# Kernel optimization log

Measured on AMD Instinct MI355X. Metric: run time of the kernel, lower is better.

## Reference

```python
import jax, jax.numpy as jnp
import numpy as np

WIRES = 4
DIM = 16  # 2**WIRES
EPS = 1e-5


def _rot_matrix(phi, theta, omega):
    # PennyLane Rot = RZ(omega) RY(theta) RZ(phi)
    c = jnp.cos(theta / 2).astype(jnp.complex64)
    s = jnp.sin(theta / 2).astype(jnp.complex64)
    ep = jnp.exp(-0.5j * (phi + omega).astype(jnp.complex64))
    em = jnp.exp(0.5j * (phi - omega).astype(jnp.complex64))
    m00 = ep * c
    m01 = -em * s
    m10 = jnp.conj(em) * s
    m11 = jnp.conj(ep) * c
    return jnp.stack([jnp.stack([m00, m01]), jnp.stack([m10, m11])])


def _apply_1q(state4, U, w):
    # state4: (B,2,2,2,2); apply 2x2 unitary on wire w (axis w+1)
    st = jnp.moveaxis(state4, w + 1, -1)
    st = st @ U.T  # sum_j st[...,j] * U[i,j]
    return jnp.moveaxis(st, -1, w + 1)


def _cnot_perm(c, t):
    # permutation of 16 basis indices for CNOT(control=c, target=t); wire 0 = MSB
    idx = np.arange(DIM)
    cbit = (idx >> (WIRES - 1 - c)) & 1
    return idx ^ (cbit << (WIRES - 1 - t))


def _circuit(x16, params):
    # AmplitudeEmbedding with normalize=True
    B = x16.shape[0]
    nrm = jnp.linalg.norm(x16, axis=1, keepdims=True)
    state = (x16 / nrm).astype(jnp.complex64)  # (B,16)
    L = params.shape[0]
    for l in range(L):
        st4 = state.reshape(B, 2, 2, 2, 2)
        for w in range(WIRES):
            U = _rot_matrix(params[l, w, 0], params[l, w, 1], params[l, w, 2])
            st4 = _apply_1q(st4, U, w)
        state = st4.reshape(B, DIM)
        r = (l % (WIRES - 1)) + 1  # StronglyEntanglingLayers default range
        for w in range(WIRES):
            perm = _cnot_perm(w, (w + r) % WIRES)
            state = state[:, perm]
    probs = (state.real ** 2 + state.imag ** 2)  # (B,16)
    p4 = probs.reshape(B, 2, 2, 2, 2)
    # <Z_w> = P(bit_w=0) - P(bit_w=1)
    outs = []
    for w in range(WIRES):
        axes = tuple(a for a in range(1, 5) if a != w + 1)
        pw = p4.sum(axis=axes)  # (B,2)
        outs.append(pw[:, 0] - pw[:, 1])
    return jnp.stack(outs, axis=1)  # (B,4)


def setup_inputs() -> dict:
    key = jax.random.key(0)
    k1, k2 = jax.random.split(key)
    B = 65536
    x = jax.random.normal(k1, (B, 1, 24, 24), dtype=jnp.float32)
    params = jax.random.normal(k2, (2, WIRES, 3), dtype=jnp.float32)
    gamma = jnp.ones((WIRES,), dtype=jnp.float32)
    beta = jnp.zeros((WIRES,), dtype=jnp.float32)
    return {"x": x, "params": params, "gamma": gamma, "beta": beta}


def reference(x, params, gamma, beta):
    B = x.shape[0]
    # avg_pool2d kernel 6: (B,1,24,24) -> (B,1,4,4) -> (B,16)
    pooled = x.reshape(B, 1, 4, 6, 4, 6).mean(axis=(3, 5)).reshape(B, DIM)
    out = _circuit(pooled, params)  # (B,4)
    # BatchNorm1d in training mode (biased batch stats)
    mu = out.mean(axis=0)
    var = ((out - mu) ** 2).mean(axis=0)
    return (out - mu) / jnp.sqrt(var + EPS) * gamma + beta
```

## Files before the change

### kernel.cpp

```cpp
#include <hip/hip_runtime.h>
#include <math.h>

#define BATCH 65536
#define XPER  576
#define NBLK  1024
#define EPB   64
#define GPI   16
#define ITERS (EPB / GPI)


__global__ __launch_bounds__(256) void circuit_kernel(
        const float* __restrict__ x, const float* __restrict__ params,
        float* __restrict__ out, float* __restrict__ accums) {
    __shared__ float sx[GPI * XPER];
    __shared__ float sU[512];
    __shared__ float sg[48];
    __shared__ float spart[8];

    const int t = threadIdx.x;
    const int e = t >> 4;
    const int p = t & 15;

    if (t < 8) {
        spart[t] = 0.0f;
        float phi   = params[t * 3 + 0];
        float theta = params[t * 3 + 1];
        float omega = params[t * 3 + 2];
        float apo = 0.5f * (phi + omega), amo = 0.5f * (phi - omega);
        sg[t * 6 + 0] = cosf(0.5f * theta);
        sg[t * 6 + 1] = sinf(0.5f * theta);
        sg[t * 6 + 2] = cosf(apo);
        sg[t * 6 + 3] = -sinf(apo);
        sg[t * 6 + 4] = cosf(amo);
        sg[t * 6 + 5] = sinf(amo);
    }
    __syncthreads();

    if (t < 16) {
        const int j = t;
        float Mr[16], Mi[16];
#pragma unroll
        for (int i = 0; i < 16; ++i) { Mr[i] = (i == j) ? 1.0f : 0.0f; Mi[i] = 0.0f; }

#pragma unroll
        for (int l = 0; l < 2; ++l) {
#pragma unroll
            for (int w = 0; w < 4; ++w) {
                const int g = l * 4 + w;
                float c   = sg[g * 6 + 0], s   = sg[g * 6 + 1];
                float epr = sg[g * 6 + 2], epi = sg[g * 6 + 3];
                float emr = sg[g * 6 + 4], emi = sg[g * 6 + 5];
                float m00r =  epr * c, m00i =  epi * c;
                float m01r = -emr * s, m01i = -emi * s;
                float m10r =  emr * s, m10i = -emi * s;
                float m11r =  epr * c, m11i = -epi * c;
                const int mask = 1 << (3 - w);
#pragma unroll
                for (int i = 0; i < 16; ++i) {
                    if (i & mask) continue;
                    int i1 = i | mask;
                    float r0 = Mr[i],  q0 = Mi[i];
                    float r1 = Mr[i1], q1 = Mi[i1];
                    Mr[i]  = m00r * r0 - m00i * q0 + m01r * r1 - m01i * q1;
                    Mi[i]  = m00r * q0 + m00i * r0 + m01r * q1 + m01i * r1;
                    Mr[i1] = m10r * r0 - m10i * q0 + m11r * r1 - m11i * q1;
                    Mi[i1] = m10r * q0 + m10i * r0 + m11r * q1 + m11i * r1;
                }
            }
            const int r = (l % 3) + 1;
#pragma unroll
            for (int w = 0; w < 4; ++w) {
                int tq = (w + r) & 3;
                int cb = 3 - w, tb = 3 - tq;
#pragma unroll
                for (int i = 0; i < 16; ++i) {
                    int pi = i ^ (((i >> cb) & 1) << tb);
                    if (pi > i) {
                        float tr = Mr[i]; Mr[i] = Mr[pi]; Mr[pi] = tr;
                        float ti = Mi[i]; Mi[i] = Mi[pi]; Mi[pi] = ti;
                    }
                }
            }
        }
#pragma unroll
        for (int i = 0; i < 16; ++i) {
            sU[i * 16 + j]       = Mr[i];
            sU[256 + i * 16 + j] = Mi[i];
        }
    }
    __syncthreads();

    float ur[16], ui[16];
    {
        const float4* u4 = (const float4*)(sU + p * 16);
        const float4* v4 = (const float4*)(sU + 256 + p * 16);
#pragma unroll
        for (int q = 0; q < 4; ++q) {
            float4 a = u4[q], b = v4[q];
            ur[4 * q + 0] = a.x; ur[4 * q + 1] = a.y; ur[4 * q + 2] = a.z; ur[4 * q + 3] = a.w;
            ui[4 * q + 0] = b.x; ui[4 * q + 1] = b.y; ui[4 * q + 2] = b.z; ui[4 * q + 3] = b.w;
        }
    }

    int c = -1;
    if      (p == 8) c = 0;
    else if (p == 4) c = 1;
    else if (p == 2) c = 2;
    else if (p == 1) c = 3;

    float accz = 0.0f, accz2 = 0.0f;
    const int base = blockIdx.x * EPB;

    for (int it = 0; it < ITERS; ++it) {
        const int ebase = base + it * GPI;
        const float4* src = (const float4*)(x + (size_t)ebase * XPER);
        float4* dst = (float4*)sx;
#pragma unroll
        for (int k = 0; k < 9; ++k) dst[k * 256 + t] = src[k * 256 + t];
        __syncthreads();

        const int r0 = (p >> 2) * 6, c0 = (p & 3) * 6;
        const float* bs = sx + e * XPER + r0 * 24 + c0;
        float sum = 0.0f;
#pragma unroll
        for (int i = 0; i < 6; ++i)
#pragma unroll
            for (int jj = 0; jj < 6; ++jj) sum += bs[i * 24 + jj];
        float v = sum * (1.0f / 36.0f);

        float n2 = v * v;
        n2 += __shfl_xor(n2, 1);
        n2 += __shfl_xor(n2, 2);
        n2 += __shfl_xor(n2, 4);
        n2 += __shfl_xor(n2, 8);

        float sr = 0.0f, si = 0.0f;
#pragma unroll
        for (int j = 0; j < 16; ++j) {
            float vj = __shfl(v, j, 16);
            sr = fmaf(ur[j], vj, sr);
            si = fmaf(ui[j], vj, si);
        }
        float prob = (sr * sr + si * si) / n2;

        float a = prob, o;
        o = __shfl_xor(a, 1); a = (t & 1) ? (o - a) : (a + o);
        o = __shfl_xor(a, 2); a = (t & 2) ? (o - a) : (a + o);
        o = __shfl_xor(a, 4); a = (t & 4) ? (o - a) : (a + o);
        o = __shfl_xor(a, 8); a = (t & 8) ? (o - a) : (a + o);

        if (c >= 0) {
            out[(size_t)(ebase + e) * 4 + c] = a;
            accz  += a;
            accz2 += a * a;
        }
        __syncthreads();
    }

    if (c >= 0) {
        atomicAdd(&spart[c], accz);
        atomicAdd(&spart[4 + c], accz2);
    }
    __syncthreads();
    if (t < 8) atomicAdd(&accums[t], spart[t]);
}

__global__ __launch_bounds__(256) void bn_apply(float* __restrict__ out,
                                                const float* __restrict__ accums,
                                                const float* __restrict__ gamma,
                                                const float* __restrict__ beta) {
    __shared__ float sc[8];
    const int t = threadIdx.x;
    if (t < 4) {
        float mu  = accums[t] * (1.0f / BATCH);
        float var = accums[4 + t] * (1.0f / BATCH) - mu * mu;
        float a = gamma[t] * rsqrtf(var + 1e-5f);
        sc[t]     = a;
        sc[4 + t] = beta[t] - mu * a;
    }
    __syncthreads();
    int i = blockIdx.x * 256 + t;
    float4 z = ((float4*)out)[i];
    z.x = fmaf(z.x, sc[0], sc[4]);
    z.y = fmaf(z.y, sc[1], sc[5]);
    z.z = fmaf(z.z, sc[2], sc[6]);
    z.w = fmaf(z.w, sc[3], sc[7]);
    ((float4*)out)[i] = z;
}

extern "C" void kernel_launch(void* const* d_in, const int* in_sizes, int n_in,
                              void* d_out, int out_size, void* d_ws, size_t ws_size,
                              hipStream_t stream) {
    const float* x      = (const float*)d_in[0];
    const float* params = (const float*)d_in[1];
    const float* gamma  = (const float*)d_in[2];
    const float* beta   = (const float*)d_in[3];
    float* out = (float*)d_out;
    float* ws  = (float*)d_ws;

    hipMemsetAsync(ws, 0, 8 * sizeof(float), stream);
    hipLaunchKernelGGL(circuit_kernel, dim3(NBLK), dim3(256), 0, stream,
                       x, params, out, ws);
    hipLaunchKernelGGL(bn_apply, dim3(BATCH / 256), dim3(256), 0, stream,
                       out, ws, gamma, beta);
}
```

Baseline: 44.97 us.

## Pool directly from global memory, 8 lanes per image, drop memset via per-block slots

Drops the shared-memory staging of input images and the per-iteration block barriers. Each lane now reads its two 6x6 pooling patches straight from global memory with float4 loads, and 8 lanes cooperate per image, each computing two rows of the 16x16 unitary product. Pooled values are exchanged through a small per-wave shared buffer instead of shuffles. BatchNorm statistics are written to per-block slots and reduced inside bn_apply, which removes the memset and the global atomics but adds a 1024-slot reduction in every bn_apply block.

```diff
diff --git a/kernel.cpp b/kernel.cpp
--- a/kernel.cpp
+++ b/kernel.cpp
@@ -4,22 +4,27 @@
 #define BATCH 65536
 #define XPER  576
 #define NBLK  1024
-#define EPB   64
-#define GPI   16
-#define ITERS (EPB / GPI)
-
-
-__global__ __launch_bounds__(256) void circuit_kernel(
+#define WPB   4
+#define RPW   2
+#define IPR   8
+
+
+__global__ __launch_bounds__(256, 3) void circuit_kernel(
         const float* __restrict__ x, const float* __restrict__ params,
-        float* __restrict__ out, float* __restrict__ accums) {
-    __shared__ float sx[GPI * XPER];
-    __shared__ float sU[512];
+        float* __restrict__ out, float* __restrict__ slots) {
+    __shared__ float sUr[16 * 20];
+    __shared__ float sUi[16 * 20];
     __shared__ float sg[48];
+    __shared__ float sv[WPB][IPR * 20];
     __shared__ float spart[8];
 
-    const int t = threadIdx.x;
-    const int e = t >> 4;
-    const int p = t & 15;
+    const int t    = threadIdx.x;
+    const int wid  = t >> 6;
+    const int lane = t & 63;
+    const int e    = lane >> 3;
+    const int q    = lane & 7;
+    const int pr   = q >> 1;
+    const int P    = q & 1;
 
     if (t < 8) {
         spart[t] = 0.0f;
@@ -41,7 +46,6 @@
         float Mr[16], Mi[16];
 #pragma unroll
         for (int i = 0; i < 16; ++i) { Mr[i] = (i == j) ? 1.0f : 0.0f; Mi[i] = 0.0f; }
-
 #pragma unroll
         for (int l = 0; l < 2; ++l) {
 #pragma unroll
@@ -67,10 +71,10 @@
                     Mi[i1] = m10r * q0 + m10i * r0 + m11r * q1 + m11i * r1;
                 }
             }
-            const int r = (l % 3) + 1;
+            const int rr = (l % 3) + 1;
 #pragma unroll
             for (int w = 0; w < 4; ++w) {
-                int tq = (w + r) & 3;
+                int tq = (w + rr) & 3;
                 int cb = 3 - w, tb = 3 - tq;
 #pragma unroll
                 for (int i = 0; i < 16; ++i) {
@@ -84,77 +88,90 @@
         }
 #pragma unroll
         for (int i = 0; i < 16; ++i) {
-            sU[i * 16 + j]       = Mr[i];
-            sU[256 + i * 16 + j] = Mi[i];
-        }
-    }
-    __syncthreads();
-
-    float ur[16], ui[16];
+            sUr[i * 20 + j] = Mr[i];
+            sUi[i * 20 + j] = Mi[i];
+        }
+    }
+    __syncthreads();
+
+    float u0r[16], u0i[16], u1r[16], u1i[16];
     {
-        const float4* u4 = (const float4*)(sU + p * 16);
-        const float4* v4 = (const float4*)(sU + 256 + p * 16);
-#pragma unroll
-        for (int q = 0; q < 4; ++q) {
-            float4 a = u4[q], b = v4[q];
-            ur[4 * q + 0] = a.x; ur[4 * q + 1] = a.y; ur[4 * q + 2] = a.z; ur[4 * q + 3] = a.w;
-            ui[4 * q + 0] = b.x; ui[4 * q + 1] = b.y; ui[4 * q + 2] = b.z; ui[4 * q + 3] = b.w;
+        const float4* r0 = (const float4*)(sUr + (2 * q) * 20);
+        const float4* r1 = (const float4*)(sUr + (2 * q + 1) * 20);
+        const float4* i0 = (const float4*)(sUi + (2 * q) * 20);
+        const float4* i1 = (const float4*)(sUi + (2 * q + 1) * 20);
+#pragma unroll
+        for (int m = 0; m < 4; ++m) {
+            float4 a = r0[m], b = r1[m], cc = i0[m], d = i1[m];
+            u0r[4*m+0]=a.x; u0r[4*m+1]=a.y; u0r[4*m+2]=a.z; u0r[4*m+3]=a.w;
+            u1r[4*m+0]=b.x; u1r[4*m+1]=b.y; u1r[4*m+2]=b.z; u1r[4*m+3]=b.w;
+            u0i[4*m+0]=cc.x; u0i[4*m+1]=cc.y; u0i[4*m+2]=cc.z; u0i[4*m+3]=cc.w;
+            u1i[4*m+0]=d.x; u1i[4*m+1]=d.y; u1i[4*m+2]=d.z; u1i[4*m+3]=d.w;
         }
     }
 
     int c = -1;
-    if      (p == 8) c = 0;
-    else if (p == 4) c = 1;
-    else if (p == 2) c = 2;
-    else if (p == 1) c = 3;
-
+    if      (q == 4) c = 0;
+    else if (q == 2) c = 1;
+    else if (q == 1) c = 2;
+    else if (q == 0) c = 3;
+
+    const int cbase = pr * 144 + P * 12;
     float accz = 0.0f, accz2 = 0.0f;
-    const int base = blockIdx.x * EPB;
-
-    for (int it = 0; it < ITERS; ++it) {
-        const int ebase = base + it * GPI;
-        const float4* src = (const float4*)(x + (size_t)ebase * XPER);
-        float4* dst = (float4*)sx;
-#pragma unroll
-        for (int k = 0; k < 9; ++k) dst[k * 256 + t] = src[k * 256 + t];
-        __syncthreads();
-
-        const int r0 = (p >> 2) * 6, c0 = (p & 3) * 6;
-        const float* bs = sx + e * XPER + r0 * 24 + c0;
-        float sum = 0.0f;
-#pragma unroll
-        for (int i = 0; i < 6; ++i)
-#pragma unroll
-            for (int jj = 0; jj < 6; ++jj) sum += bs[i * 24 + jj];
-        float v = sum * (1.0f / 36.0f);
-
-        float n2 = v * v;
-        n2 += __shfl_xor(n2, 1);
-        n2 += __shfl_xor(n2, 2);
-        n2 += __shfl_xor(n2, 4);
-        n2 += __shfl_xor(n2, 8);
-
-        float sr = 0.0f, si = 0.0f;
+
+#pragma unroll
+    for (int rd = 0; rd < RPW; ++rd) {
+        const size_t img = (size_t)blockIdx.x * 64 + wid * 16 + rd * 8 + e;
+        const float* ip = x + img * XPER + cbase;
+
+        float L = 0.0f, R = 0.0f;
+#pragma unroll
+        for (int r = 0; r < 6; ++r) {
+            float4 a = *(const float4*)(ip + r * 24);
+            float4 b = *(const float4*)(ip + r * 24 + 4);
+            float4 d = *(const float4*)(ip + r * 24 + 8);
+            L += a.x + a.y + a.z + a.w + b.x + b.y;
+            R += b.z + b.w + d.x + d.y + d.z + d.w;
+        }
+        float vL = L * (1.0f / 36.0f), vR = R * (1.0f / 36.0f);
+
+        *(float2*)(&sv[wid][e * 20 + 2 * q]) = make_float2(vL, vR);
+        float vv[16];
+        {
+            const float4* vb = (const float4*)(&sv[wid][e * 20]);
+#pragma unroll
+            for (int m = 0; m < 4; ++m) {
+                float4 a = vb[m];
+                vv[4*m+0]=a.x; vv[4*m+1]=a.y; vv[4*m+2]=a.z; vv[4*m+3]=a.w;
+            }
+        }
+
+        float n2 = 0.0f, sr0 = 0.0f, si0 = 0.0f, sr1 = 0.0f, si1 = 0.0f;
 #pragma unroll
         for (int j = 0; j < 16; ++j) {
-            float vj = __shfl(v, j, 16);
-            sr = fmaf(ur[j], vj, sr);
-            si = fmaf(ui[j], vj, si);
-        }
-        float prob = (sr * sr + si * si) / n2;
-
-        float a = prob, o;
-        o = __shfl_xor(a, 1); a = (t & 1) ? (o - a) : (a + o);
-        o = __shfl_xor(a, 2); a = (t & 2) ? (o - a) : (a + o);
-        o = __shfl_xor(a, 4); a = (t & 4) ? (o - a) : (a + o);
-        o = __shfl_xor(a, 8); a = (t & 8) ? (o - a) : (a + o);
+            float vj = vv[j];
+            n2  = fmaf(vj, vj, n2);
+            sr0 = fmaf(u0r[j], vj, sr0); si0 = fmaf(u0i[j], vj, si0);
+            sr1 = fmaf(u1r[j], vj, sr1); si1 = fmaf(u1i[j], vj, si1);
+        }
+        float inv = 1.0f / n2;
+        float p0 = (sr0 * sr0 + si0 * si0) * inv;
+        float p1 = (sr1 * sr1 + si1 * si1) * inv;
+
+        float u = p0 + p1, d = p0 - p1, o;
+        o = __shfl_xor(u, 1); u = (q & 1) ? (o - u) : (u + o);
+        o = __shfl_xor(u, 2); u = (q & 2) ? (o - u) : (u + o);
+        o = __shfl_xor(u, 4); u = (q & 4) ? (o - u) : (u + o);
+        d += __shfl_xor(d, 1);
+        d += __shfl_xor(d, 2);
+        d += __shfl_xor(d, 4);
 
         if (c >= 0) {
-            out[(size_t)(ebase + e) * 4 + c] = a;
-            accz  += a;
-            accz2 += a * a;
-        }
-        __syncthreads();
+            float z = (q == 0) ? d : u;
+            out[img * 4 + c] = z;
+            accz  += z;
+            accz2 += z * z;
+        }
     }
 
     if (c >= 0) {
@@ -162,18 +179,31 @@
         atomicAdd(&spart[4 + c], accz2);
     }
     __syncthreads();
-    if (t < 8) atomicAdd(&accums[t], spart[t]);
+    if (t < 8) slots[blockIdx.x * 8 + t] = spart[t];
 }
 
 __global__ __launch_bounds__(256) void bn_apply(float* __restrict__ out,
-                                                const float* __restrict__ accums,
+                                                const float* __restrict__ slots,
                                                 const float* __restrict__ gamma,
                                                 const float* __restrict__ beta) {
+    __shared__ float red[256];
     __shared__ float sc[8];
     const int t = threadIdx.x;
+    const int ch = t & 7, g = t >> 3;
+    float s = 0.0f;
+#pragma unroll
+    for (int k = 0; k < NBLK / 32; ++k)
+        s += slots[(size_t)(g + 32 * k) * 8 + ch];
+    red[t] = s;
+    __syncthreads();
+#pragma unroll
+    for (int stp = 128; stp >= 8; stp >>= 1) {
+        if (t < stp) red[t] += red[t + stp];
+        __syncthreads();
+    }
     if (t < 4) {
-        float mu  = accums[t] * (1.0f / BATCH);
-        float var = accums[4 + t] * (1.0f / BATCH) - mu * mu;
+        float mu  = red[t] * (1.0f / BATCH);
+        float var = red[4 + t] * (1.0f / BATCH) - mu * mu;
         float a = gamma[t] * rsqrtf(var + 1e-5f);
         sc[t]     = a;
         sc[4 + t] = beta[t] - mu * a;
@@ -198,7 +228,6 @@
     float* out = (float*)d_out;
     float* ws  = (float*)d_ws;
 
-    hipMemsetAsync(ws, 0, 8 * sizeof(float), stream);
     hipLaunchKernelGGL(circuit_kernel, dim3(NBLK), dim3(256), 0, stream,
                        x, params, out, ws);
     hipLaunchKernelGGL(bn_apply, dim3(BATCH / 256), dim3(256), 0, stream,
```

Result: faster. 36.05 us (median of 2 runs) (-19.8%).
